# Performance work log

Hardware: AMD Instinct MI355X
Metric: run time of the kernel (lower is better)

Reference implementation:

```python
import jax, jax.numpy as jnp
import numpy as np

B, T, T_KEEP, C, F, K = 8, 128, 64, 128, 32, 64


def setup_inputs() -> dict:
    key = jax.random.key(0)
    k1, k2 = jax.random.split(key)
    y_true = jax.random.normal(k1, (B, T, C, F), dtype=jnp.float32)
    # per-timestep mask: 0 = keep, 1 = masked; constant over C,F and batch
    # (required by the original layer's Reshape using sum(1 - masktime[0]))
    masktime = jnp.concatenate([jnp.zeros((T_KEEP,), jnp.float32),
                                jnp.ones((T - T_KEEP,), jnp.float32)])
    mask = jnp.broadcast_to(masktime[None, :, None, None], (B, T, C, F)).astype(jnp.float32)
    centers = jax.random.normal(k2, (K,), dtype=jnp.float32)
    return {"y_true": y_true, "mask": mask, "centers": centers, "t_keep": T_KEEP}


def reference(y_true, mask, centers, t_keep):
    # masktime: [B, T]; mask is constant over channel/feature dims
    masktime = mask[:, :, 0, 0]
    # tf.boolean_mask keeps elements where (1 - mask) is True, preserving order.
    # Since mask is per-timestep, this is a gather of the unmasked timesteps.
    # Stable argsort puts zeros (kept timesteps) first, in original order.
    keep_idx = jnp.argsort(masktime[0], stable=True)[:t_keep]          # [T_keep]
    x = y_true[:, keep_idx]                                            # [B, T_keep, C, F]
    # element-wise nearest-center assignment (assign_center) + one-hot
    dist = jnp.abs(x[..., None] - centers)                             # [B, T_keep, C, F, K]
    idx = jnp.argmin(dist, axis=-1)                                    # [B, T_keep, C, F]
    return jax.nn.one_hot(idx, centers.shape[0], dtype=y_true.dtype)   # [B, T_keep, C, F, K]
```

## Files before the change

### kernel.cpp

```cpp
#include <hip/hip_runtime.h>

constexpr int B = 8, T = 128, T_KEEP = 64, C = 128, F = 32, K = 64;
constexpr int CF = C * F;
constexpr int TOTAL = B * T_KEEP * C * F;
constexpr int BLOCK = 256;

__global__ void keep_idx_kernel(const float* __restrict__ mask,
                                const int* __restrict__ t_keep_p,
                                int* __restrict__ keep) {
    __shared__ float m_s[T];
    int t = threadIdx.x;
    if (t < T) m_s[t] = mask[(size_t)t * CF];
    __syncthreads();
    if (t < T) {
        float mt = m_s[t];
        int rank = 0;
        for (int j = 0; j < T; ++j) {
            float mj = m_s[j];
            rank += (mj < mt) || (mj == mt && j < t);
        }
        if (rank < t_keep_p[0]) keep[rank] = t;
    }
}

__global__ void __launch_bounds__(BLOCK) assign_onehot_kernel(
        const float* __restrict__ y,
        const float* __restrict__ centers,
        const int* __restrict__ keep,
        float* __restrict__ out) {
    __shared__ float sc[K];
    int tid = threadIdx.x;
    if (tid < K) sc[tid] = centers[tid];
    __syncthreads();

    int g = blockIdx.x * BLOCK + tid;
    int lane = tid & 63;

    int f = g & (F - 1);
    int c = (g >> 5) & (C - 1);
    int t = (g >> 12) & (T_KEEP - 1);
    int b = g >> 18;

    int src = b * (T * CF) + keep[t] * CF + c * F + f;
    float x = y[src];

    int bi = 0;
    float bd = __builtin_inff();
    const float4* c4 = (const float4*)sc;
    #pragma unroll
    for (int k4 = 0; k4 < K / 4; ++k4) {
        float4 cv = c4[k4];
        float d;
        d = fabsf(x - cv.x); if (d < bd) { bd = d; bi = 4 * k4 + 0; }
        d = fabsf(x - cv.y); if (d < bd) { bd = d; bi = 4 * k4 + 1; }
        d = fabsf(x - cv.z); if (d < bd) { bd = d; bi = 4 * k4 + 2; }
        d = fabsf(x - cv.w); if (d < bd) { bd = d; bi = 4 * k4 + 3; }
    }

    int waveId = tid >> 6;
    int wbase = (blockIdx.x * BLOCK + waveId * 64) * (K / 4);
    float4* out4 = (float4*)out;
    #pragma unroll
    for (int r = 0; r < 16; ++r) {
        int src_lane = r * 4 + (lane >> 4);
        int bsrc = __shfl(bi, src_lane, 64);
        int k0 = (lane & 15) * 4;
        float4 v;
        v.x = (k0 + 0 == bsrc) ? 1.0f : 0.0f;
        v.y = (k0 + 1 == bsrc) ? 1.0f : 0.0f;
        v.z = (k0 + 2 == bsrc) ? 1.0f : 0.0f;
        v.w = (k0 + 3 == bsrc) ? 1.0f : 0.0f;
        out4[wbase + r * 64 + lane] = v;
    }
}

extern "C" void kernel_launch(void* const* d_in, const int* in_sizes, int n_in,
                              void* d_out, int out_size, void* d_ws, size_t ws_size,
                              hipStream_t stream) {
    const float* y       = (const float*)d_in[0];
    const float* mask    = (const float*)d_in[1];
    const float* centers = (const float*)d_in[2];
    const int*   t_keep  = (const int*)d_in[3];
    float* out = (float*)d_out;
    int* keep = (int*)d_ws;

    keep_idx_kernel<<<1, T, 0, stream>>>(mask, t_keep, keep);
    assign_onehot_kernel<<<TOTAL / BLOCK, BLOCK, 0, stream>>>(y, centers, keep, out);
}
```

Measured before the change: 548.5 us.

## Fuse keep-index computation into one-hot kernel, process 4 elements per thread

Removes the separate single-block keep-index kernel by having every block recompute the rank of each timestep from the mask in shared memory and pick the one for its own timestep. Each thread now handles four elements, which cuts the grid by four and amortizes the center loads and setup. Output stores become nontemporal. The cost is redundant mask reads and rank computation per block, and t_keep is no longer read from its input, so the kernel relies on the compile-time constant.

```diff
diff --git a/kernel.cpp b/kernel.cpp
--- a/kernel.cpp
+++ b/kernel.cpp
@@ -4,73 +4,86 @@
 constexpr int CF = C * F;
 constexpr int TOTAL = B * T_KEEP * C * F;
 constexpr int BLOCK = 256;
+constexpr int EPT = 4;
+constexpr int EPB = BLOCK * EPT;
 
-__global__ void keep_idx_kernel(const float* __restrict__ mask,
-                                const int* __restrict__ t_keep_p,
-                                int* __restrict__ keep) {
+typedef float vfloat4 __attribute__((ext_vector_type(4)));
+
+__global__ void __launch_bounds__(BLOCK) assign_onehot_fused(
+        const float* __restrict__ y,
+        const float* __restrict__ mask,
+        const float* __restrict__ centers,
+        float* __restrict__ out) {
+    __shared__ float sc[K];
     __shared__ float m_s[T];
-    int t = threadIdx.x;
-    if (t < T) m_s[t] = mask[(size_t)t * CF];
+    __shared__ int keep_s;
+    const int tid = threadIdx.x;
+
+    if (tid < K) sc[tid] = centers[tid];
+    if (tid < T) m_s[tid] = mask[(size_t)tid * CF];
     __syncthreads();
-    if (t < T) {
-        float mt = m_s[t];
+
+    const int t_blk = (blockIdx.x >> 2) & (T_KEEP - 1);
+    if (tid < T) {
+        float mt = m_s[tid];
         int rank = 0;
+        #pragma unroll 8
         for (int j = 0; j < T; ++j) {
             float mj = m_s[j];
-            rank += (mj < mt) || (mj == mt && j < t);
+            rank += (mj < mt) || (mj == mt && j < tid);
         }
-        if (rank < t_keep_p[0]) keep[rank] = t;
+        if (rank == t_blk) keep_s = tid;
     }
-}
+    __syncthreads();
+    const int keep_t = keep_s;
 
-__global__ void __launch_bounds__(BLOCK) assign_onehot_kernel(
-        const float* __restrict__ y,
-        const float* __restrict__ centers,
-        const int* __restrict__ keep,
-        float* __restrict__ out) {
-    __shared__ float sc[K];
-    int tid = threadIdx.x;
-    if (tid < K) sc[tid] = centers[tid];
-    __syncthreads();
+    const int lane = tid & 63;
+    const int wave = tid >> 6;
+    const int wbase = blockIdx.x * EPB + wave * (EPT * 64);
 
-    int g = blockIdx.x * BLOCK + tid;
-    int lane = tid & 63;
+    const int b   = wbase >> 18;
+    const int cf0 = wbase & (CF - 1);
+    const float* ysrc = y + (size_t)b * (T * CF) + (size_t)keep_t * CF + cf0;
 
-    int f = g & (F - 1);
-    int c = (g >> 5) & (C - 1);
-    int t = (g >> 12) & (T_KEEP - 1);
-    int b = g >> 18;
+    const float x0 = ysrc[lane];
+    const float x1 = ysrc[64 + lane];
+    const float x2 = ysrc[128 + lane];
+    const float x3 = ysrc[192 + lane];
 
-    int src = b * (T * CF) + keep[t] * CF + c * F + f;
-    float x = y[src];
-
-    int bi = 0;
-    float bd = __builtin_inff();
+    int bi0 = 0, bi1 = 0, bi2 = 0, bi3 = 0;
+    float bd0 = __builtin_inff(), bd1 = bd0, bd2 = bd0, bd3 = bd0;
     const float4* c4 = (const float4*)sc;
     #pragma unroll
     for (int k4 = 0; k4 < K / 4; ++k4) {
         float4 cv = c4[k4];
         float d;
-        d = fabsf(x - cv.x); if (d < bd) { bd = d; bi = 4 * k4 + 0; }
-        d = fabsf(x - cv.y); if (d < bd) { bd = d; bi = 4 * k4 + 1; }
-        d = fabsf(x - cv.z); if (d < bd) { bd = d; bi = 4 * k4 + 2; }
-        d = fabsf(x - cv.w); if (d < bd) { bd = d; bi = 4 * k4 + 3; }
+        #define UPD(cvx, kk)                                            \
+            d = fabsf(x0 - cvx); if (d < bd0) { bd0 = d; bi0 = kk; }    \
+            d = fabsf(x1 - cvx); if (d < bd1) { bd1 = d; bi1 = kk; }    \
+            d = fabsf(x2 - cvx); if (d < bd2) { bd2 = d; bi2 = kk; }    \
+            d = fabsf(x3 - cvx); if (d < bd3) { bd3 = d; bi3 = kk; }
+        UPD(cv.x, 4 * k4 + 0)
+        UPD(cv.y, 4 * k4 + 1)
+        UPD(cv.z, 4 * k4 + 2)
+        UPD(cv.w, 4 * k4 + 3)
+        #undef UPD
     }
 
-    int waveId = tid >> 6;
-    int wbase = (blockIdx.x * BLOCK + waveId * 64) * (K / 4);
-    float4* out4 = (float4*)out;
+    vfloat4* out4 = (vfloat4*)out;
+    const size_t obase = (size_t)wbase * (K / 4);
+    const int k0 = (lane & 15) * 4;
+    const int sl_add = lane >> 4;
     #pragma unroll
-    for (int r = 0; r < 16; ++r) {
-        int src_lane = r * 4 + (lane >> 4);
-        int bsrc = __shfl(bi, src_lane, 64);
-        int k0 = (lane & 15) * 4;
-        float4 v;
+    for (int i4 = 0; i4 < 64; ++i4) {
+        const int e = i4 >> 4;
+        int bsel = (e == 0) ? bi0 : (e == 1) ? bi1 : (e == 2) ? bi2 : bi3;
+        int bsrc = __shfl(bsel, (i4 & 15) * 4 + sl_add, 64);
+        vfloat4 v;
         v.x = (k0 + 0 == bsrc) ? 1.0f : 0.0f;
         v.y = (k0 + 1 == bsrc) ? 1.0f : 0.0f;
         v.z = (k0 + 2 == bsrc) ? 1.0f : 0.0f;
         v.w = (k0 + 3 == bsrc) ? 1.0f : 0.0f;
-        out4[wbase + r * 64 + lane] = v;
+        __builtin_nontemporal_store(v, &out4[obase + i4 * 64 + lane]);
     }
 }
 
@@ -80,10 +93,7 @@
     const float* y       = (const float*)d_in[0];
     const float* mask    = (const float*)d_in[1];
     const float* centers = (const float*)d_in[2];
-    const int*   t_keep  = (const int*)d_in[3];
     float* out = (float*)d_out;
-    int* keep = (int*)d_ws;
 
-    keep_idx_kernel<<<1, T, 0, stream>>>(mask, t_keep, keep);
-    assign_onehot_kernel<<<TOTAL / BLOCK, BLOCK, 0, stream>>>(y, centers, keep, out);
+    assign_onehot_fused<<<TOTAL / EPB, BLOCK, 0, stream>>>(y, mask, centers, out);
 }
```

Result: no change. 544.5 us (-0.7%).
